# Optimization experiments

Measured on AMD Instinct MI355X. Metric: run time of the kernel, lower is better.

The kernel has to match this reference:

```python
import jax, jax.numpy as jnp
import numpy as np


def setup_inputs() -> dict:
    key = jax.random.key(0)
    kq, kk, kv = jax.random.split(key, 3)
    B, H, N, D = 4, 16, 4096, 64
    E = 64
    # q, k are positive (random-feature kernel outputs in Performer)
    q = jax.random.uniform(kq, (B, H, N, D), dtype=jnp.float32)
    k = jax.random.uniform(kk, (B, H, N, D), dtype=jnp.float32)
    v = jax.random.normal(kv, (B, H, N, E), dtype=jnp.float32)
    return {"q": q, "k": k, "v": v}


def reference(q, k, v):
    # k_cumsum: sum of keys over sequence dim -> [B, H, D]
    k_cumsum = k.sum(axis=-2)
    # D_inv: per-query normalizer -> [B, H, N]
    D_inv = 1.0 / jnp.einsum('bhnd,bhd->bhn', q, k_cumsum)
    # context: k^T v -> [B, H, D, E]
    context = jnp.einsum('bhnd,bhne->bhde', k, v)
    # out: context applied to q, normalized -> [B, H, N, E]
    out = jnp.einsum('bhde,bhnd,bhn->bhne', context, q, D_inv)
    return out
```

## Files before the change

### kernel.cpp

```cpp
#include <hip/hip_runtime.h>


namespace {

constexpr int kBH = 64;
constexpr int kN  = 4096;
constexpr int kD  = 64;
constexpr int kE  = 64;

using frag_ab = __attribute__((ext_vector_type(8))) short;
using frag_cd = __attribute__((ext_vector_type(4))) float;

__device__ __forceinline__ short f2bf(float f) {
  unsigned u = __float_as_uint(f);
  u += 0x7FFF + ((u >> 16) & 1);
  return (short)(u >> 16);
}

__global__ __launch_bounds__(256) void fa_phaseA(
    const float* __restrict__ k, const float* __restrict__ v,
    float* __restrict__ ctxp, float* __restrict__ ksump, int nc)
{
  const int bid = blockIdx.x;
  const int bh = bid / nc;
  const int chunk = bid - bh * nc;
  const int chunkLen = kN / nc;
  const float* kbase = k + ((size_t)bh * kN + (size_t)chunk * chunkLen) * kD;
  const float* vbase = v + ((size_t)bh * kN + (size_t)chunk * chunkLen) * kE;

  const int tid = threadIdx.x;
  const int w = tid >> 6;
  const int lane = tid & 63;
  const int r = lane & 15;
  const int g = lane >> 4;

  frag_cd acc[4];
  #pragma unroll
  for (int et = 0; et < 4; ++et) acc[et] = frag_cd{0.f, 0.f, 0.f, 0.f};
  float ksp = 0.f;

  const int nsteps = chunkLen / 32;
  for (int s = 0; s < nsteps; ++s) {
    const int n0 = s * 32 + 8 * g;
    const float* pa = kbase + (size_t)n0 * kD + 16 * w + r;
    const float* pb = vbase + (size_t)n0 * kE + r;

    float ka[8];
    #pragma unroll
    for (int b = 0; b < 8; ++b) ka[b] = pa[b * 64];
    float vb[4][8];
    #pragma unroll
    for (int et = 0; et < 4; ++et)
      #pragma unroll
      for (int b = 0; b < 8; ++b) vb[et][b] = pb[et * 16 + b * 64];

    frag_ab af;
    #pragma unroll
    for (int b = 0; b < 8; ++b) { af[b] = f2bf(ka[b]); ksp += ka[b]; }
    #pragma unroll
    for (int et = 0; et < 4; ++et) {
      frag_ab bf;
      #pragma unroll
      for (int b = 0; b < 8; ++b) bf[b] = f2bf(vb[et][b]);
      acc[et] = __builtin_amdgcn_mfma_f32_16x16x32_bf16(af, bf, acc[et], 0, 0, 0);
    }
  }

  ksp += __shfl_xor(ksp, 16);
  ksp += __shfl_xor(ksp, 32);
  if (lane < 16) ksump[(size_t)bid * kD + 16 * w + lane] = ksp;

  float* cdst = ctxp + (size_t)bid * kD * kE;
  #pragma unroll
  for (int et = 0; et < 4; ++et)
    #pragma unroll
    for (int reg = 0; reg < 4; ++reg)
      cdst[(size_t)(16 * w + 4 * g + reg) * kE + 16 * et + r] = acc[et][reg];
}

__global__ __launch_bounds__(256) void fa_phaseB(
    const float* __restrict__ ctxp, const float* __restrict__ ksump,
    short* __restrict__ ctxT, short* __restrict__ ksumb, int nc)
{
  const int t = blockIdx.x * 256 + threadIdx.x;
  if (blockIdx.x < 256) {
    const int head = t >> 10;
    const int i = t & 1023;
    const int e = i >> 4;
    const int d0 = (i & 15) * 4;
    const float* src = ctxp + (size_t)head * nc * (kD * kE) + e;
    float s0 = 0.f, s1 = 0.f, s2 = 0.f, s3 = 0.f;
    for (int c = 0; c < nc; ++c) {
      const float* p = src + (size_t)c * (kD * kE);
      s0 += p[(d0 + 0) * kE]; s1 += p[(d0 + 1) * kE];
      s2 += p[(d0 + 2) * kE]; s3 += p[(d0 + 3) * kE];
    }
    short* dst = ctxT + (size_t)head * (kD * kE) + e * kD + d0;
    int lo = (unsigned short)f2bf(s0) | ((unsigned)(unsigned short)f2bf(s1) << 16);
    int hi = (unsigned short)f2bf(s2) | ((unsigned)(unsigned short)f2bf(s3) << 16);
    *(int2*)dst = make_int2(lo, hi);
  } else {
    const int t2 = t - 256 * 256;
    if (t2 >= kBH * 16) return;
    const int head = t2 >> 4;
    const int d0 = (t2 & 15) * 4;
    const float* src = ksump + (size_t)head * nc * kD + d0;
    float s[4] = {0.f, 0.f, 0.f, 0.f};
    for (int c = 0; c < nc; ++c) {
      const float* p = src + (size_t)c * kD;
      s[0] += p[0]; s[1] += p[1]; s[2] += p[2]; s[3] += p[3];
    }
    short* dst = ksumb + (size_t)head * kD + d0;
    int lo = (unsigned short)f2bf(s[0]) | ((unsigned)(unsigned short)f2bf(s[1]) << 16);
    int hi = (unsigned short)f2bf(s[2]) | ((unsigned)(unsigned short)f2bf(s[3]) << 16);
    *(int2*)dst = make_int2(lo, hi);
  }
}

__global__ __launch_bounds__(256) void fa_phaseC(
    const float* __restrict__ q, const short* __restrict__ ctxT,
    const short* __restrict__ ksumb, float* __restrict__ out)
{
  const int bid = blockIdx.x;
  const int bh = bid >> 5;
  const int tile = bid & 31;
  const int tid = threadIdx.x;
  const int w = tid >> 6;
  const int lane = tid & 63;
  const int r = lane & 15;
  const int g = lane >> 4;
  const int rowb = tile * 128 + w * 32;

  const float* qb = q + ((size_t)bh * kN + rowb) * kD;
  const short* cb = ctxT + (size_t)bh * kD * kE;
  const short* kb = ksumb + (size_t)bh * kD;

  frag_ab B[4][2];
  #pragma unroll
  for (int et = 0; et < 4; ++et)
    #pragma unroll
    for (int ks = 0; ks < 2; ++ks)
      B[et][ks] = *(const frag_ab*)(cb + (size_t)(16 * et + r) * kD + 32 * ks + 8 * g);

  const frag_ab zero8 = frag_ab{0, 0, 0, 0, 0, 0, 0, 0};
  frag_ab Bk[2];
  #pragma unroll
  for (int ks = 0; ks < 2; ++ks) {
    frag_ab t = *(const frag_ab*)(kb + 32 * ks + 8 * g);
    Bk[ks] = (r == 0) ? t : zero8;
  }

  frag_ab A[2][2];
  #pragma unroll
  for (int rt = 0; rt < 2; ++rt)
    #pragma unroll
    for (int ks = 0; ks < 2; ++ks) {
      const float* pq = qb + (size_t)(16 * rt + r) * kD + 32 * ks + 8 * g;
      const float4 lo = *(const float4*)pq;
      const float4 hi = *(const float4*)(pq + 4);
      frag_ab a;
      a[0] = f2bf(lo.x); a[1] = f2bf(lo.y); a[2] = f2bf(lo.z); a[3] = f2bf(lo.w);
      a[4] = f2bf(hi.x); a[5] = f2bf(hi.y); a[6] = f2bf(hi.z); a[7] = f2bf(hi.w);
      A[rt][ks] = a;
    }

  frag_cd acc[2][4];
  frag_cd dacc[2];
  #pragma unroll
  for (int rt = 0; rt < 2; ++rt) {
    dacc[rt] = frag_cd{0.f, 0.f, 0.f, 0.f};
    #pragma unroll
    for (int et = 0; et < 4; ++et) acc[rt][et] = frag_cd{0.f, 0.f, 0.f, 0.f};
  }

  #pragma unroll
  for (int rt = 0; rt < 2; ++rt)
    #pragma unroll
    for (int ks = 0; ks < 2; ++ks) {
      #pragma unroll
      for (int et = 0; et < 4; ++et)
        acc[rt][et] =
            __builtin_amdgcn_mfma_f32_16x16x32_bf16(A[rt][ks], B[et][ks], acc[rt][et], 0, 0, 0);
      dacc[rt] =
          __builtin_amdgcn_mfma_f32_16x16x32_bf16(A[rt][ks], Bk[ks], dacc[rt], 0, 0, 0);
    }

  float* ob = out + ((size_t)bh * kN + rowb) * kE;
  #pragma unroll
  for (int rt = 0; rt < 2; ++rt) {
    float inv[4];
    #pragma unroll
    for (int reg = 0; reg < 4; ++reg) {
      const float dv = __shfl(dacc[rt][reg], lane & 48);
      inv[reg] = 1.0f / dv;
    }
    #pragma unroll
    for (int et = 0; et < 4; ++et)
      #pragma unroll
      for (int reg = 0; reg < 4; ++reg)
        ob[(size_t)(16 * rt + 4 * g + reg) * kE + 16 * et + r] = acc[rt][et][reg] * inv[reg];
  }
}

}

extern "C" void kernel_launch(void* const* d_in, const int* in_sizes, int n_in,
                              void* d_out, int out_size, void* d_ws, size_t ws_size,
                              hipStream_t stream) {
  const float* q = (const float*)d_in[0];
  const float* k = (const float*)d_in[1];
  const float* v = (const float*)d_in[2];
  float* out = (float*)d_out;

  int nc = 16;
  auto need = [](int c) {
    return (size_t)(kBH * (size_t)c * (kD * kE + kD)) * sizeof(float) +
           (size_t)(kBH * (kD * kE + kD)) * sizeof(short);
  };
  while (nc > 1 && need(nc) > ws_size) nc >>= 1;

  float* ctxp  = (float*)d_ws;
  float* ksump = ctxp + (size_t)kBH * nc * kD * kE;
  short* ctxT  = (short*)(ksump + (size_t)kBH * nc * kD);
  short* ksumb = ctxT + (size_t)kBH * kD * kE;

  fa_phaseA<<<dim3(kBH * nc), dim3(256), 0, stream>>>(k, v, ctxp, ksump, nc);
  fa_phaseB<<<dim3(260), dim3(256), 0, stream>>>(ctxp, ksump, ctxT, ksumb, nc);
  fa_phaseC<<<dim3(kBH * 32), dim3(256), 0, stream>>>(q, ctxT, ksumb, out);
}
```

Baseline: 239.3 us.

## Stage K and V through double-buffered LDS transpose in context accumulation

```diff
diff --git a/kernel.cpp b/kernel.cpp
--- a/kernel.cpp
+++ b/kernel.cpp
@@ -7,6 +7,7 @@
 constexpr int kN  = 4096;
 constexpr int kD  = 64;
 constexpr int kE  = 64;
+constexpr int kLS = 40;
 
 using frag_ab = __attribute__((ext_vector_type(8))) short;
 using frag_cd = __attribute__((ext_vector_type(4))) float;
@@ -15,6 +16,9 @@
   unsigned u = __float_as_uint(f);
   u += 0x7FFF + ((u >> 16) & 1);
   return (short)(u >> 16);
+}
+__device__ __forceinline__ int pack2(float a, float b) {
+  return (int)(unsigned short)f2bf(a) | ((int)(unsigned short)f2bf(b) << 16);
 }
 
 __global__ __launch_bounds__(256) void fa_phaseA(
@@ -33,42 +37,63 @@
   const int lane = tid & 63;
   const int r = lane & 15;
   const int g = lane >> 4;
+  const int u = tid & 15;
+  const int p = tid >> 4;
+
+  __shared__ __align__(16) short skT[2][64 * kLS];
+  __shared__ __align__(16) short svT[2][64 * kLS];
 
   frag_cd acc[4];
   #pragma unroll
   for (int et = 0; et < 4; ++et) acc[et] = frag_cd{0.f, 0.f, 0.f, 0.f};
-  float ksp = 0.f;
-
-  const int nsteps = chunkLen / 32;
-  for (int s = 0; s < nsteps; ++s) {
-    const int n0 = s * 32 + 8 * g;
-    const float* pa = kbase + (size_t)n0 * kD + 16 * w + r;
-    const float* pb = vbase + (size_t)n0 * kE + r;
-
-    float ka[8];
-    #pragma unroll
-    for (int b = 0; b < 8; ++b) ka[b] = pa[b * 64];
-    float vb[4][8];
-    #pragma unroll
-    for (int et = 0; et < 4; ++et)
-      #pragma unroll
-      for (int b = 0; b < 8; ++b) vb[et][b] = pb[et * 16 + b * 64];
-
-    frag_ab af;
-    #pragma unroll
-    for (int b = 0; b < 8; ++b) { af[b] = f2bf(ka[b]); ksp += ka[b]; }
-    #pragma unroll
-    for (int et = 0; et < 4; ++et) {
-      frag_ab bf;
-      #pragma unroll
-      for (int b = 0; b < 8; ++b) bf[b] = f2bf(vb[et][b]);
-      acc[et] = __builtin_amdgcn_mfma_f32_16x16x32_bf16(af, bf, acc[et], 0, 0, 0);
-    }
-  }
-
-  ksp += __shfl_xor(ksp, 16);
-  ksp += __shfl_xor(ksp, 32);
-  if (lane < 16) ksump[(size_t)bid * kD + 16 * w + lane] = ksp;
+  frag_cd dacc = frag_cd{0.f, 0.f, 0.f, 0.f};
+  frag_ab ones;
+  #pragma unroll
+  for (int i = 0; i < 8; ++i) ones[i] = (short)0x3F80;
+
+  float4 rk0, rk1, rv0, rv1;
+  auto loadrows = [&](int s) {
+    const float* kp = kbase + ((size_t)s * 32 + 2 * p) * kD + 4 * u;
+    const float* vp = vbase + ((size_t)s * 32 + 2 * p) * kE + 4 * u;
+    rk0 = *(const float4*)kp;        rk1 = *(const float4*)(kp + kD);
+    rv0 = *(const float4*)vp;        rv1 = *(const float4*)(vp + kE);
+  };
+  auto writebuf = [&](int b) {
+    short* kt = &skT[b][0];
+    short* vt = &svT[b][0];
+    const float k0[4] = {rk0.x, rk0.y, rk0.z, rk0.w};
+    const float k1[4] = {rk1.x, rk1.y, rk1.z, rk1.w};
+    const float v0[4] = {rv0.x, rv0.y, rv0.z, rv0.w};
+    const float v1[4] = {rv1.x, rv1.y, rv1.z, rv1.w};
+    #pragma unroll
+    for (int i = 0; i < 4; ++i) {
+      *(int*)(kt + (4 * u + i) * kLS + 2 * p) = pack2(k0[i], k1[i]);
+      *(int*)(vt + (4 * u + i) * kLS + 2 * p) = pack2(v0[i], v1[i]);
+    }
+  };
+
+  const int nsub = chunkLen / 32;
+  loadrows(0);
+  writebuf(0);
+  int cur = 0;
+  for (int s = 0; s < nsub; ++s) {
+    __syncthreads();
+    if (s + 1 < nsub) loadrows(s + 1);
+    const short* kt = &skT[cur][0];
+    const short* vt = &svT[cur][0];
+    const frag_ab A  = *(const frag_ab*)(kt + (16 * w + r) * kLS + 8 * g);
+    const frag_ab B0 = *(const frag_ab*)(vt + (r)           * kLS + 8 * g);
+    const frag_ab B1 = *(const frag_ab*)(vt + (16 + r)      * kLS + 8 * g);
+    const frag_ab B2 = *(const frag_ab*)(vt + (32 + r)      * kLS + 8 * g);
+    const frag_ab B3 = *(const frag_ab*)(vt + (48 + r)      * kLS + 8 * g);
+    acc[0] = __builtin_amdgcn_mfma_f32_16x16x32_bf16(A, B0, acc[0], 0, 0, 0);
+    acc[1] = __builtin_amdgcn_mfma_f32_16x16x32_bf16(A, B1, acc[1], 0, 0, 0);
+    acc[2] = __builtin_amdgcn_mfma_f32_16x16x32_bf16(A, B2, acc[2], 0, 0, 0);
+    acc[3] = __builtin_amdgcn_mfma_f32_16x16x32_bf16(A, B3, acc[3], 0, 0, 0);
+    dacc   = __builtin_amdgcn_mfma_f32_16x16x32_bf16(A, ones, dacc, 0, 0, 0);
+    if (s + 1 < nsub) writebuf(cur ^ 1);
+    cur ^= 1;
+  }
 
   float* cdst = ctxp + (size_t)bid * kD * kE;
   #pragma unroll
@@ -76,6 +101,11 @@
     #pragma unroll
     for (int reg = 0; reg < 4; ++reg)
       cdst[(size_t)(16 * w + 4 * g + reg) * kE + 16 * et + r] = acc[et][reg];
+  if (r == 0) {
+    #pragma unroll
+    for (int reg = 0; reg < 4; ++reg)
+      ksump[(size_t)bid * kD + 16 * w + 4 * g + reg] = dacc[reg];
+  }
 }
 
 __global__ __launch_bounds__(256) void fa_phaseB(
@@ -91,14 +121,12 @@
     const float* src = ctxp + (size_t)head * nc * (kD * kE) + e;
     float s0 = 0.f, s1 = 0.f, s2 = 0.f, s3 = 0.f;
     for (int c = 0; c < nc; ++c) {
-      const float* p = src + (size_t)c * (kD * kE);
-      s0 += p[(d0 + 0) * kE]; s1 += p[(d0 + 1) * kE];
-      s2 += p[(d0 + 2) * kE]; s3 += p[(d0 + 3) * kE];
+      const float* ptr = src + (size_t)c * (kD * kE);
+      s0 += ptr[(d0 + 0) * kE]; s1 += ptr[(d0 + 1) * kE];
+      s2 += ptr[(d0 + 2) * kE]; s3 += ptr[(d0 + 3) * kE];
     }
     short* dst = ctxT + (size_t)head * (kD * kE) + e * kD + d0;
-    int lo = (unsigned short)f2bf(s0) | ((unsigned)(unsigned short)f2bf(s1) << 16);
-    int hi = (unsigned short)f2bf(s2) | ((unsigned)(unsigned short)f2bf(s3) << 16);
-    *(int2*)dst = make_int2(lo, hi);
+    *(int2*)dst = make_int2(pack2(s0, s1), pack2(s2, s3));
   } else {
     const int t2 = t - 256 * 256;
     if (t2 >= kBH * 16) return;
@@ -107,13 +135,11 @@
     const float* src = ksump + (size_t)head * nc * kD + d0;
     float s[4] = {0.f, 0.f, 0.f, 0.f};
     for (int c = 0; c < nc; ++c) {
-      const float* p = src + (size_t)c * kD;
-      s[0] += p[0]; s[1] += p[1]; s[2] += p[2]; s[3] += p[3];
+      const float* ptr = src + (size_t)c * kD;
+      s[0] += ptr[0]; s[1] += ptr[1]; s[2] += ptr[2]; s[3] += ptr[3];
     }
     short* dst = ksumb + (size_t)head * kD + d0;
-    int lo = (unsigned short)f2bf(s[0]) | ((unsigned)(unsigned short)f2bf(s[1]) << 16);
-    int hi = (unsigned short)f2bf(s[2]) | ((unsigned)(unsigned short)f2bf(s[3]) << 16);
-    *(int2*)dst = make_int2(lo, hi);
+    *(int2*)dst = make_int2(pack2(s[0], s[1]), pack2(s[2], s[3]));
   }
 }
 
```

Result: faster. 234.4 us (-2.0%).
